# Optimization experiments

Measured on AMD Instinct MI355X. Metric: run time of the kernel, lower is better.

Reference implementation:

```python
import jax, jax.numpy as jnp
import numpy as np

N_EMBD = 2048
HEAD_SIZE = 128

def setup_inputs() -> dict:
    key = jax.random.key(0)
    kx, kk, kq, kv = jax.random.split(key, 4)
    bound = 1.0 / np.sqrt(N_EMBD)  # torch Linear default init range
    x = jax.random.normal(kx, (4, 4096, N_EMBD), dtype=jnp.float32)
    Wk = jax.random.uniform(kk, (N_EMBD, HEAD_SIZE), jnp.float32, -bound, bound)
    Wq = jax.random.uniform(kq, (N_EMBD, HEAD_SIZE), jnp.float32, -bound, bound)
    Wv = jax.random.uniform(kv, (N_EMBD, HEAD_SIZE), jnp.float32, -bound, bound)
    return {"x": x, "Wk": Wk, "Wq": Wq, "Wv": Wv}

def reference(x, Wk, Wq, Wv):
    B, T, C = x.shape
    k = jnp.einsum('btc,ch->bth', x, Wk)
    q = jnp.einsum('btc,ch->bth', x, Wq)
    v = jnp.einsum('btc,ch->bth', x, Wv)
    # NOTE: original scales by C**-0.5 where C = n_embd (input dim), not head_size
    scores = jnp.einsum('bth,bsh->bts', q, k) * (C ** -0.5)
    causal = jnp.tril(jnp.ones((T, T), dtype=bool))  # [T,T]
    scores = jnp.where(causal, scores, -jnp.inf)
    probs = jax.nn.softmax(scores, axis=-1)
    # dropout_probability = 0.0 -> identity
    return jnp.einsum('bts,bsh->bth', probs, v)
```

## Files before the change

### kernel.cpp

```cpp
#include <hip/hip_runtime.h>
#include <hip/hip_bf16.h>

#define T_SEQ 4096
#define NB 4
#define CEMB 2048
#define HS 128

typedef __attribute__((ext_vector_type(8))) short bf16x8;
typedef __attribute__((ext_vector_type(4))) float f32x4;
typedef __attribute__((ext_vector_type(16))) float f32x16;

__device__ inline short f2bf(float f) {
    union { float f; unsigned u; } v; v.f = f;
    unsigned r = v.u + 0x7FFFu + ((v.u >> 16) & 1u);
    return (short)(r >> 16);
}

__device__ inline unsigned pk2(float lo, float hi) {
    unsigned r;
    asm("v_cvt_pk_bf16_f32 %0, %1, %2" : "=v"(r) : "v"(lo), "v"(hi));
    return r;
}

__device__ inline void gld16(const void* gsrc, void* lds) {
    __builtin_amdgcn_global_load_lds(
        (const __attribute__((address_space(1))) unsigned*)gsrc,
        (__attribute__((address_space(3))) unsigned*)lds, 16, 0, 0);
}

__global__ __launch_bounds__(256) void wt_kernel(
    const float* __restrict__ Wq, const float* __restrict__ Wk,
    const float* __restrict__ Wv, short* __restrict__ Wt) {
    int d = blockIdx.x * 256 + threadIdx.x;
    int mat = d >> 18;
    int rm  = d & 262143;
    int s   = rm >> 13;
    int e   = rm & 8191;
    int p   = e * 2;
    int n   = p >> 7;
    int lin = p ^ ((n & 7) << 4);
    int kk  = (lin & 127) >> 1;
    int k   = s * 64 + kk;
    const float* W = (mat == 0) ? Wq : (mat == 1) ? Wk : Wv;
    Wt[d] = f2bf(W[k * HS + n]);
}

__global__ __launch_bounds__(256, 3) void proj_kernel(
    const float* __restrict__ x, const short* __restrict__ Wt,
    short* __restrict__ qg, short* __restrict__ kg, short* __restrict__ vtg) {
    __shared__ short Wlds[3][8192];

    const int tid = threadIdx.x;
    const int w   = tid >> 6;
    const int l   = tid & 63;
    const int lg  = l >> 4;
    const int lr  = l & 15;

    const int bid = blockIdx.x;
    const int wk  = (bid & 7) * 96 + (bid >> 3);
    const int mat = wk % 3;
    const int m0  = (wk / 3) * 64;

    const short* Wp = Wt + (long)mat * 262144;

    f32x4 acc[8];
    #pragma unroll
    for (int b = 0; b < 8; b++) acc[b] = (f32x4){0.f, 0.f, 0.f, 0.f};

    const float* xrow = x + (long)(m0 + w * 16 + lr) * CEMB;
    const int sw = (lr & 7) << 4;

    float4 xs[3][4];

#define STAGE(S, B) do {                                                   \
        const short* gp_ = Wp + (long)(S) * 8192 + (long)(w * 4) * 512 + l * 8; \
        gld16(gp_,        &Wlds[B][(w * 4 + 0) * 512]);                    \
        gld16(gp_ + 512,  &Wlds[B][(w * 4 + 1) * 512]);                    \
        gld16(gp_ + 1024, &Wlds[B][(w * 4 + 2) * 512]);                    \
        gld16(gp_ + 1536, &Wlds[B][(w * 4 + 3) * 512]);                    \
    } while (0)

#define LOADX(S, B) do {                                                   \
        const float* xn_ = xrow + (S) * 64;                                \
        xs[B][0] = *reinterpret_cast<const float4*>(xn_ + lg * 8);         \
        xs[B][1] = *reinterpret_cast<const float4*>(xn_ + lg * 8 + 4);     \
        xs[B][2] = *reinterpret_cast<const float4*>(xn_ + 32 + lg * 8);    \
        xs[B][3] = *reinterpret_cast<const float4*>(xn_ + 32 + lg * 8 + 4);\
    } while (0)

    STAGE(0, 0);
    LOADX(0, 0);
    STAGE(1, 1);
    LOADX(1, 1);

#define STEP(S, B0, B2) do {                                               \
        asm volatile("s_waitcnt vmcnt(8) lgkmcnt(0)\n\ts_barrier" ::: "memory"); \
        if ((S) + 2 < 32) { STAGE((S) + 2, B2); LOADX((S) + 2, B2); }      \
        bf16x8 a0, a1;                                                     \
        a0[0] = f2bf(xs[B0][0].x); a0[1] = f2bf(xs[B0][0].y);              \
        a0[2] = f2bf(xs[B0][0].z); a0[3] = f2bf(xs[B0][0].w);              \
        a0[4] = f2bf(xs[B0][1].x); a0[5] = f2bf(xs[B0][1].y);              \
        a0[6] = f2bf(xs[B0][1].z); a0[7] = f2bf(xs[B0][1].w);              \
        a1[0] = f2bf(xs[B0][2].x); a1[1] = f2bf(xs[B0][2].y);              \
        a1[2] = f2bf(xs[B0][2].z); a1[3] = f2bf(xs[B0][2].w);              \
        a1[4] = f2bf(xs[B0][3].x); a1[5] = f2bf(xs[B0][3].y);              \
        a1[6] = f2bf(xs[B0][3].z); a1[7] = f2bf(xs[B0][3].w);              \
        const char* lbase_ = (const char*)&Wlds[B0][0];                    \
        _Pragma("unroll")                                                  \
        for (int nt = 0; nt < 8; nt++) {                                   \
            int off_ = (((nt * 16 + lr) * 128 + lg * 16)) ^ sw;            \
            bf16x8 bfr_ = *reinterpret_cast<const bf16x8*>(lbase_ + off_); \
            acc[nt] = __builtin_amdgcn_mfma_f32_16x16x32_bf16(             \
                a0, bfr_, acc[nt], 0, 0, 0);                               \
        }                                                                  \
        _Pragma("unroll")                                                  \
        for (int nt = 0; nt < 8; nt++) {                                   \
            int off_ = (((nt * 16 + lr) * 128 + lg * 16 + 64)) ^ sw;       \
            bf16x8 bfr_ = *reinterpret_cast<const bf16x8*>(lbase_ + off_); \
            acc[nt] = __builtin_amdgcn_mfma_f32_16x16x32_bf16(             \
                a1, bfr_, acc[nt], 0, 0, 0);                               \
        }                                                                  \
    } while (0)

    for (int s = 0; s < 30; s += 3) {
        STEP(s, 0, 2);
        STEP(s + 1, 1, 0);
        STEP(s + 2, 2, 1);
    }
    STEP(30, 0, 2);
    STEP(31, 1, 0);

#undef STEP
#undef LOADX
#undef STAGE

    if (mat == 0) {
        const float scale = 0.0318793851f;
        #pragma unroll
        for (int nt = 0; nt < 8; nt++)
            #pragma unroll
            for (int r = 0; r < 4; r++) {
                int row = m0 + w * 16 + lg * 4 + r;
                qg[(long)row * HS + nt * 16 + lr] = f2bf(acc[nt][r] * scale);
            }
    } else if (mat == 1) {
        #pragma unroll
        for (int nt = 0; nt < 8; nt++)
            #pragma unroll
            for (int r = 0; r < 4; r++) {
                int row = m0 + w * 16 + lg * 4 + r;
                kg[(long)row * HS + nt * 16 + lr] = f2bf(acc[nt][r]);
            }
    } else {
        #pragma unroll
        for (int nt = 0; nt < 8; nt++)
            #pragma unroll
            for (int r = 0; r < 4; r++) {
                int row = m0 + w * 16 + lg * 4 + r;
                int b   = row >> 12;
                int tl  = row & 4095;
                vtg[(long)b * (HS * T_SEQ) + (long)(nt * 16 + lr) * T_SEQ + tl]
                    = f2bf(acc[nt][r]);
            }
    }
}

__global__ __launch_bounds__(256, 2) void attn_kernel(
    const short* __restrict__ qg, const short* __restrict__ kg,
    const short* __restrict__ vtg, float* __restrict__ out) {
    __shared__ float Lacc[4][32][128];
    __shared__ float Lm[4][32];
    __shared__ float Ll[4][32];

    const int tid = threadIdx.x;
    const int w   = tid >> 6;
    const int l   = tid & 63;
    const int c31 = l & 31;
    const int hi  = l >> 5;
    const int hi4 = hi << 2;
    const int hi8 = hi << 3;

    const int bid = blockIdx.x;
    const int xcd = bid & 7;
    const int idx = bid >> 3;
    const int b   = xcd >> 1;
    const int qt  = 127 - ((idx << 1) | (xcd & 1));
    const int q0  = qt * 32;
    const int qrow = q0 + c31;

    const short* kb = kg  + (long)b * T_SEQ * HS;
    const short* vb = vtg + (long)b * HS * T_SEQ;
    const short* qb = qg  + (long)(b * T_SEQ + qrow) * HS;

    f32x16 accO[4];
    #pragma unroll
    for (int nb = 0; nb < 4; nb++)
        #pragma unroll
        for (int i = 0; i < 16; i++) accO[nb][i] = 0.f;
    float mrow = -__builtin_inff();
    float lsum = 0.f;

    const int ntk = (qt >> 1) + 1;

    #pragma unroll 1
    for (int t = w; t < ntk; t += 4) {
        const int kv0 = t * 64;

        bf16x8 ka[8], kb2[8];
        #pragma unroll
        for (int kc = 0; kc < 8; kc++)
            ka[kc] = *reinterpret_cast<const bf16x8*>(
                &kb[(long)(kv0 + c31) * HS + kc * 16 + hi8]);
        #pragma unroll
        for (int kc = 0; kc < 8; kc++)
            kb2[kc] = *reinterpret_cast<const bf16x8*>(
                &kb[(long)(kv0 + 32 + c31) * HS + kc * 16 + hi8]);

        bf16x8 qf[8];
        #pragma unroll
        for (int kc = 0; kc < 8; kc++)
            qf[kc] = *reinterpret_cast<const bf16x8*>(&qb[kc * 16 + hi8]);

        bf16x8 vfA[2][4];
        #pragma unroll
        for (int kc = 0; kc < 2; kc++)
            #pragma unroll
            for (int nb = 0; nb < 4; nb++)
                vfA[kc][nb] = *reinterpret_cast<const bf16x8*>(
                    &vb[(long)(nb * 32 + c31) * T_SEQ + kv0 + kc * 16 + hi8]);

        f32x16 SA, SB;
        #pragma unroll
        for (int i = 0; i < 16; i++) { SA[i] = 0.f; SB[i] = 0.f; }
        __builtin_amdgcn_s_setprio(1);
        #pragma unroll
        for (int kc = 0; kc < 8; kc++) {
            SA = __builtin_amdgcn_mfma_f32_32x32x16_bf16(ka[kc],  qf[kc], SA, 0, 0, 0);
            SB = __builtin_amdgcn_mfma_f32_32x32x16_bf16(kb2[kc], qf[kc], SB, 0, 0, 0);
        }
        __builtin_amdgcn_s_setprio(0);

        float pA[16], pB[16];
        #pragma unroll
        for (int r = 0; r < 16; r++) { pA[r] = SA[r]; pB[r] = SB[r]; }

        if (kv0 + 63 > q0) {
            #pragma unroll
            for (int r = 0; r < 16; r++) {
                int kr = kv0 + (r & 3) + 8 * (r >> 2) + hi4;
                pA[r] = (kr > qrow)      ? -__builtin_inff() : pA[r];
                pB[r] = (kr + 32 > qrow) ? -__builtin_inff() : pB[r];
            }
        }

        float t16[16];
        #pragma unroll
        for (int r = 0; r < 16; r++) t16[r] = fmaxf(pA[r], pB[r]);
        #pragma unroll
        for (int s2 = 8; s2 >= 1; s2 >>= 1)
            #pragma unroll
            for (int r = 0; r < 8; r++)
                if (r < s2) t16[r] = fmaxf(t16[r], t16[r + s2]);
        float mt = fmaxf(t16[0], __shfl_xor(t16[0], 32));

        if (__any(mt > mrow)) {
            float mnew = fmaxf(mrow, mt);
            float fac  = exp2f(mrow - mnew);
            lsum *= fac;
            #pragma unroll
            for (int nb = 0; nb < 4; nb++)
                #pragma unroll
                for (int i = 0; i < 16; i++) accO[nb][i] *= fac;
            mrow = mnew;
        }

        bf16x8 vfB[2][4];
        #pragma unroll
        for (int kc = 0; kc < 2; kc++)
            #pragma unroll
            for (int nb = 0; nb < 4; nb++)
                vfB[kc][nb] = *reinterpret_cast<const bf16x8*>(
                    &vb[(long)(nb * 32 + c31) * T_SEQ + kv0 + (kc + 2) * 16 + hi8]);

        #pragma unroll
        for (int r = 0; r < 16; r++) {
            pA[r] = exp2f(pA[r] - mrow);
            pB[r] = exp2f(pB[r] - mrow);
        }
        float s16[16];
        #pragma unroll
        for (int r = 0; r < 16; r++) s16[r] = pA[r] + pB[r];
        #pragma unroll
        for (int s2 = 8; s2 >= 1; s2 >>= 1)
            #pragma unroll
            for (int r = 0; r < 8; r++)
                if (r < s2) s16[r] += s16[r + s2];
        lsum += s16[0] + __shfl_xor(s16[0], 32);

        bf16x8 pf[4];
        #pragma unroll
        for (int kc = 0; kc < 4; kc++) {
            const int V0 = 2 * kc, V1 = 2 * kc + 1;
            const int r0 = ((V0 >> 2) << 4) | ((V0 & 3) << 2);
            const int r1 = ((V1 >> 2) << 4) | ((V1 & 3) << 2);
#define PSEL(i) ((i) < 16 ? pA[(i) & 15] : pB[(i) & 15])
            unsigned a0 = pk2(PSEL(r0 + 0), PSEL(r0 + 1));
            unsigned a1 = pk2(PSEL(r0 + 2), PSEL(r0 + 3));
            unsigned b0 = pk2(PSEL(r1 + 0), PSEL(r1 + 1));
            unsigned b1 = pk2(PSEL(r1 + 2), PSEL(r1 + 3));
#undef PSEL
            unsigned k0 = hi ? b0 : a0, k1 = hi ? b1 : a1;
            unsigned s0 = hi ? a0 : b0, s1 = hi ? a1 : b1;
            unsigned g0 = (unsigned)__shfl_xor((int)s0, 32);
            unsigned g1 = (unsigned)__shfl_xor((int)s1, 32);
            union { unsigned u[4]; bf16x8 v; } U;
            U.u[0] = hi ? g0 : k0;
            U.u[1] = hi ? g1 : k1;
            U.u[2] = hi ? k0 : g0;
            U.u[3] = hi ? k1 : g1;
            pf[kc] = U.v;
        }

        __builtin_amdgcn_s_setprio(1);
        #pragma unroll
        for (int nb = 0; nb < 4; nb++)
            accO[nb] = __builtin_amdgcn_mfma_f32_32x32x16_bf16(pf[0], vfA[0][nb], accO[nb], 0, 0, 0);
        #pragma unroll
        for (int nb = 0; nb < 4; nb++)
            accO[nb] = __builtin_amdgcn_mfma_f32_32x32x16_bf16(pf[1], vfA[1][nb], accO[nb], 0, 0, 0);
        #pragma unroll
        for (int nb = 0; nb < 4; nb++)
            accO[nb] = __builtin_amdgcn_mfma_f32_32x32x16_bf16(pf[2], vfB[0][nb], accO[nb], 0, 0, 0);
        #pragma unroll
        for (int nb = 0; nb < 4; nb++)
            accO[nb] = __builtin_amdgcn_mfma_f32_32x32x16_bf16(pf[3], vfB[1][nb], accO[nb], 0, 0, 0);
        __builtin_amdgcn_s_setprio(0);
    }

    #pragma unroll
    for (int nb = 0; nb < 4; nb++)
        #pragma unroll
        for (int r = 0; r < 16; r++)
            Lacc[w][(r & 3) + 8 * (r >> 2) + hi4][nb * 32 + c31] = accO[nb][r];
    if (l < 32) { Lm[w][c31] = mrow; Ll[w][c31] = lsum; }
    __syncthreads();

    {
        const int row = tid >> 3;
        const int c0  = (tid & 7) * 16;
        float m0 = Lm[0][row], m1 = Lm[1][row], m2 = Lm[2][row], m3 = Lm[3][row];
        float ms = fmaxf(fmaxf(m0, m1), fmaxf(m2, m3));
        float f0 = exp2f(m0 - ms), f1 = exp2f(m1 - ms);
        float f2 = exp2f(m2 - ms), f3 = exp2f(m3 - ms);
        float L = Ll[0][row] * f0 + Ll[1][row] * f1 + Ll[2][row] * f2 + Ll[3][row] * f3;
        float inv = 1.0f / L;
        float* op = &out[((long)b * T_SEQ + q0 + row) * HS + c0];
        #pragma unroll
        for (int j = 0; j < 16; j++) {
            float o = Lacc[0][row][c0 + j] * f0 + Lacc[1][row][c0 + j] * f1
                    + Lacc[2][row][c0 + j] * f2 + Lacc[3][row][c0 + j] * f3;
            op[j] = o * inv;
        }
    }
}

extern "C" void kernel_launch(void* const* d_in, const int* in_sizes, int n_in,
                              void* d_out, int out_size, void* d_ws, size_t ws_size,
                              hipStream_t stream) {
    const float* x  = (const float*)d_in[0];
    const float* Wk = (const float*)d_in[1];
    const float* Wq = (const float*)d_in[2];
    const float* Wv = (const float*)d_in[3];
    float* out = (float*)d_out;

    char* ws = (char*)d_ws;
    short* Wt  = (short*)ws;
    short* qg  = (short*)(ws + 1572864);
    short* kg  = (short*)(ws + 1572864 + 4194304);
    short* vtg = (short*)(ws + 1572864 + 8388608);

    wt_kernel  <<<3072, 256, 0, stream>>>(Wq, Wk, Wv, Wt);
    proj_kernel<<<768,  256, 0, stream>>>(x, Wt, qg, kg, vtg);
    attn_kernel<<<512,  256, 0, stream>>>(qg, kg, vtg, out);
}
```

Measured before the change: 162.1 us.

## Stage K tiles into swizzled LDS via async loads, hoist Q fragment load

```diff
diff --git a/kernel.cpp b/kernel.cpp
--- a/kernel.cpp
+++ b/kernel.cpp
@@ -144,12 +144,14 @@
                 qg[(long)row * HS + nt * 16 + lr] = f2bf(acc[nt][r] * scale);
             }
     } else if (mat == 1) {
+        short* kt = kg + ((long)(m0 >> 6)) * 8192;
         #pragma unroll
         for (int nt = 0; nt < 8; nt++)
             #pragma unroll
             for (int r = 0; r < 4; r++) {
-                int row = m0 + w * 16 + lg * 4 + r;
-                kg[(long)row * HS + nt * 16 + lr] = f2bf(acc[nt][r]);
+                int r64  = w * 16 + lg * 4 + r;
+                int byte = (r64 * 256 + (nt * 16 + lr) * 2) ^ ((r64 & 7) << 4);
+                kt[byte >> 1] = f2bf(acc[nt][r]);
             }
     } else {
         #pragma unroll
@@ -168,7 +170,7 @@
 __global__ __launch_bounds__(256, 2) void attn_kernel(
     const short* __restrict__ qg, const short* __restrict__ kg,
     const short* __restrict__ vtg, float* __restrict__ out) {
-    __shared__ float Lacc[4][32][128];
+    __shared__ __align__(16) char pool[65536];
     __shared__ float Lm[4][32];
     __shared__ float Ll[4][32];
 
@@ -188,9 +190,23 @@
     const int q0  = qt * 32;
     const int qrow = q0 + c31;
 
-    const short* kb = kg  + (long)b * T_SEQ * HS;
-    const short* vb = vtg + (long)b * HS * T_SEQ;
-    const short* qb = qg  + (long)(b * T_SEQ + qrow) * HS;
+    const short* kbimg = kg + (long)b * 64 * 8192;
+    const short* vb    = vtg + (long)b * HS * T_SEQ;
+
+    short* Kw = (short*)(pool + (w << 14));
+
+#define STAGEK(TILE) do {                                                  \
+        const short* gp_ = kbimg + (long)(TILE) * 8192 + l * 8;            \
+        _Pragma("unroll")                                                  \
+        for (int i = 0; i < 16; i++)                                       \
+            gld16(gp_ + i * 512, Kw + i * 512 + l * 8);                    \
+    } while (0)
+
+    bf16x8 qf[8];
+    #pragma unroll
+    for (int kc = 0; kc < 8; kc++)
+        qf[kc] = *reinterpret_cast<const bf16x8*>(
+            &qg[(long)(b * T_SEQ + qrow) * HS + kc * 16 + hi8]);
 
     f32x16 accO[4];
     #pragma unroll
@@ -202,24 +218,17 @@
 
     const int ntk = (qt >> 1) + 1;
 
+    STAGEK(w);
+
+    const int swz = (c31 & 7) << 4;
+    const int rbA = c31 * 256;
+    const int rbB = (32 + c31) * 256;
+
     #pragma unroll 1
     for (int t = w; t < ntk; t += 4) {
         const int kv0 = t * 64;
 
-        bf16x8 ka[8], kb2[8];
-        #pragma unroll
-        for (int kc = 0; kc < 8; kc++)
-            ka[kc] = *reinterpret_cast<const bf16x8*>(
-                &kb[(long)(kv0 + c31) * HS + kc * 16 + hi8]);
-        #pragma unroll
-        for (int kc = 0; kc < 8; kc++)
-            kb2[kc] = *reinterpret_cast<const bf16x8*>(
-                &kb[(long)(kv0 + 32 + c31) * HS + kc * 16 + hi8]);
-
-        bf16x8 qf[8];
-        #pragma unroll
-        for (int kc = 0; kc < 8; kc++)
-            qf[kc] = *reinterpret_cast<const bf16x8*>(&qb[kc * 16 + hi8]);
+        asm volatile("s_waitcnt vmcnt(0)" ::: "memory");
 
         bf16x8 vfA[2][4];
         #pragma unroll
@@ -235,10 +244,17 @@
         __builtin_amdgcn_s_setprio(1);
         #pragma unroll
         for (int kc = 0; kc < 8; kc++) {
-            SA = __builtin_amdgcn_mfma_f32_32x32x16_bf16(ka[kc],  qf[kc], SA, 0, 0, 0);
-            SB = __builtin_amdgcn_mfma_f32_32x32x16_bf16(kb2[kc], qf[kc], SB, 0, 0, 0);
+            const int cb = kc * 32 + hi * 16;
+            bf16x8 ka = *reinterpret_cast<const bf16x8*>(
+                (const char*)Kw + ((rbA + cb) ^ swz));
+            bf16x8 kb2 = *reinterpret_cast<const bf16x8*>(
+                (const char*)Kw + ((rbB + cb) ^ swz));
+            SA = __builtin_amdgcn_mfma_f32_32x32x16_bf16(ka,  qf[kc], SA, 0, 0, 0);
+            SB = __builtin_amdgcn_mfma_f32_32x32x16_bf16(kb2, qf[kc], SB, 0, 0, 0);
         }
         __builtin_amdgcn_s_setprio(0);
+
+        if (t + 4 < ntk) STAGEK(t + 4);
 
         float pA[16], pB[16];
         #pragma unroll
@@ -336,13 +352,17 @@
             accO[nb] = __builtin_amdgcn_mfma_f32_32x32x16_bf16(pf[3], vfB[1][nb], accO[nb], 0, 0, 0);
         __builtin_amdgcn_s_setprio(0);
     }
-
-    #pragma unroll
-    for (int nb = 0; nb < 4; nb++)
-        #pragma unroll
-        for (int r = 0; r < 16; r++)
-            Lacc[w][(r & 3) + 8 * (r >> 2) + hi4][nb * 32 + c31] = accO[nb][r];
-    if (l < 32) { Lm[w][c31] = mrow; Ll[w][c31] = lsum; }
+#undef STAGEK
+
+    {
+        float* LaccW = (float*)(pool + (w << 14));
+        #pragma unroll
+        for (int nb = 0; nb < 4; nb++)
+            #pragma unroll
+            for (int r = 0; r < 16; r++)
+                LaccW[((r & 3) + 8 * (r >> 2) + hi4) * 128 + nb * 32 + c31] = accO[nb][r];
+        if (l < 32) { Lm[w][c31] = mrow; Ll[w][c31] = lsum; }
+    }
     __syncthreads();
 
     {
@@ -355,10 +375,14 @@
         float L = Ll[0][row] * f0 + Ll[1][row] * f1 + Ll[2][row] * f2 + Ll[3][row] * f3;
         float inv = 1.0f / L;
         float* op = &out[((long)b * T_SEQ + q0 + row) * HS + c0];
+        const float* L0 = (const float*)(pool);
+        const float* L1 = (const float*)(pool + 16384);
+        const float* L2 = (const float*)(pool + 32768);
+        const float* L3 = (const float*)(pool + 49152);
         #pragma unroll
         for (int j = 0; j < 16; j++) {
-            float o = Lacc[0][row][c0 + j] * f0 + Lacc[1][row][c0 + j] * f1
-                    + Lacc[2][row][c0 + j] * f2 + Lacc[3][row][c0 + j] * f3;
+            float o = L0[row * 128 + c0 + j] * f0 + L1[row * 128 + c0 + j] * f1
+                    + L2[row * 128 + c0 + j] * f2 + L3[row * 128 + c0 + j] * f3;
             op[j] = o * inv;
         }
     }
```

Result: faster. 132.7 us (-18.1%).
